# Kernel tuning notes

Measured on AMD Instinct MI355X. Metric: run time of the kernel, lower is better.

The kernel has to match this reference:

```python
import jax, jax.numpy as jnp
import numpy as np

N_NODES = 500_000
N_Q = 500_000
H = 8       # heads
MH = 8      # m // heads


def setup_inputs() -> dict:
    key = jax.random.key(0)
    ks = jax.random.split(key, 6)
    q_phi = jax.random.normal(ks[0], (N_Q, H, MH), dtype=jnp.float32)
    phi_k_pos = jax.random.normal(ks[1], (H, MH, N_NODES), dtype=jnp.float32)
    phi_k_neg = jax.random.normal(ks[2], (H, MH, N_NODES), dtype=jnp.float32)
    # degrees are nonnegative counts accumulated in build(); simulate with scaled uniforms
    deg_pos = jax.random.uniform(ks[3], (N_NODES, H), dtype=jnp.float32) * 32.0
    deg_neg = jax.random.uniform(ks[4], (N_NODES, H), dtype=jnp.float32) * 32.0
    k_indices = jax.random.randint(ks[5], (N_Q,), 0, N_NODES)
    return {
        "q_phi": q_phi,
        "phi_k_pos": phi_k_pos,
        "phi_k_neg": phi_k_neg,
        "deg_pos": deg_pos,
        "deg_neg": deg_neg,
        "k_indices": k_indices,
    }


def reference(q_phi, phi_k_pos, phi_k_neg, deg_pos, deg_neg, k_indices):
    # gather cached per-node random-feature sums: [h, mh, Nq] -> [Nq, h, mh]
    pk_pos = jnp.transpose(phi_k_pos[:, :, k_indices], (2, 0, 1))
    pk_neg = jnp.transpose(phi_k_neg[:, :, k_indices], (2, 0, 1))
    # per-head dot product over the feature chunk
    num_pos = jnp.sum(q_phi * pk_pos, axis=-1)  # [Nq, h]
    num_neg = jnp.sum(q_phi * pk_neg, axis=-1)  # [Nq, h]
    # degree-normalize with clamp_min(1)
    den_pos = jnp.maximum(deg_pos[k_indices], 1.0)  # [Nq, h]
    den_neg = jnp.maximum(deg_neg[k_indices], 1.0)
    return (num_pos / den_pos, num_neg / den_neg)
```

## Files before the change

### kernel.cpp

```cpp
#include <hip/hip_runtime.h>
#include <hip/hip_bf16.h>

constexpr int N_NODES = 500000;
constexpr int N_Q     = 500000;
constexpr int H       = 8;
constexpr int FEAT    = 64;
constexpr int TILES   = (N_NODES + 63) / 64;

__global__ __launch_bounds__(256) void transpose_pk(
    const float* __restrict__ pk_pos,
    const float* __restrict__ pk_neg,
    float* __restrict__ dst)
{
    __shared__ float lds[64 * 65];
    const int t  = threadIdx.x;
    const int n0 = blockIdx.x * 64;
    const float* src = blockIdx.y ? pk_neg : pk_pos;
    float* d = dst + (size_t)blockIdx.y * (size_t)N_NODES * FEAT;

    {
        const int  n  = t & 63;
        const bool ok = (n0 + n) < N_NODES;
        for (int f = (t >> 6); f < 64; f += 4)
            lds[f * 65 + n] = ok ? src[(size_t)f * N_NODES + n0 + n] : 0.0f;
    }
    __syncthreads();
    {
        const int f  = t & 63;
        const int nb = (t >> 6) * 16;
        for (int r = 0; r < 16; ++r) {
            const int n = nb + r;
            if (n0 + n < N_NODES)
                d[(size_t)(n0 + n) * FEAT + f] = lds[f * 65 + n];
        }
    }
}

__global__ __launch_bounds__(256, 4) void iskde_main_kernel(
    const float* __restrict__ q_phi,
    const float* __restrict__ pk_t,
    const float* __restrict__ deg_pos,
    const float* __restrict__ deg_neg,
    const int*   __restrict__ k_idx,
    float*       __restrict__ out)
{
    const int wave_in_blk = threadIdx.x >> 6;
    const int lane        = threadIdx.x & 63;
    const int q           = blockIdx.x * 4 + wave_in_blk;
    if (q >= N_Q) return;

    const int j = k_idx[q];

    const float qv = q_phi[(size_t)q * FEAT + lane];
    const float pv = pk_t[(size_t)j * FEAT + lane];
    const float nv = pk_t[(size_t)(N_NODES + j) * FEAT + lane];

    float sp = qv * pv;
    float sn = qv * nv;

    sp += __shfl_xor(sp, 1, 64);
    sn += __shfl_xor(sn, 1, 64);
    sp += __shfl_xor(sp, 2, 64);
    sn += __shfl_xor(sn, 2, 64);
    sp += __shfl_xor(sp, 4, 64);
    sn += __shfl_xor(sn, 4, 64);

    if ((lane & 7) == 0) {
        const int h = lane >> 3;
        const float dp = fmaxf(deg_pos[(size_t)j * H + h], 1.0f);
        const float dn = fmaxf(deg_neg[(size_t)j * H + h], 1.0f);
        const size_t o = (size_t)q * H + h;
        out[o]                   = sp / dp;
        out[(size_t)N_Q * H + o] = sn / dn;
    }
}

__global__ __launch_bounds__(256, 4) void iskde_gather_kernel(
    const float* __restrict__ q_phi,
    const float* __restrict__ pk_pos,
    const float* __restrict__ pk_neg,
    const float* __restrict__ deg_pos,
    const float* __restrict__ deg_neg,
    const int*   __restrict__ k_idx,
    float*       __restrict__ out)
{
    const int wave_in_blk = threadIdx.x >> 6;
    const int lane        = threadIdx.x & 63;
    const int q           = blockIdx.x * 4 + wave_in_blk;
    if (q >= N_Q) return;

    const int j = k_idx[q];
    const float qv = q_phi[(size_t)q * FEAT + lane];
    const size_t col = (size_t)lane * (size_t)N_NODES + (size_t)j;
    const float pv = pk_pos[col];
    const float nv = pk_neg[col];

    float sp = qv * pv;
    float sn = qv * nv;
    sp += __shfl_xor(sp, 1, 64);
    sn += __shfl_xor(sn, 1, 64);
    sp += __shfl_xor(sp, 2, 64);
    sn += __shfl_xor(sn, 2, 64);
    sp += __shfl_xor(sp, 4, 64);
    sn += __shfl_xor(sn, 4, 64);

    if ((lane & 7) == 0) {
        const int h = lane >> 3;
        const float dp = fmaxf(deg_pos[(size_t)j * H + h], 1.0f);
        const float dn = fmaxf(deg_neg[(size_t)j * H + h], 1.0f);
        const size_t o = (size_t)q * H + h;
        out[o]                   = sp / dp;
        out[(size_t)N_Q * H + o] = sn / dn;
    }
}

extern "C" void kernel_launch(void* const* d_in, const int* in_sizes, int n_in,
                              void* d_out, int out_size, void* d_ws, size_t ws_size,
                              hipStream_t stream) {
    const float* q_phi   = (const float*)d_in[0];
    const float* pk_pos  = (const float*)d_in[1];
    const float* pk_neg  = (const float*)d_in[2];
    const float* deg_pos = (const float*)d_in[3];
    const float* deg_neg = (const float*)d_in[4];
    const int*   k_idx   = (const int*)d_in[5];
    float*       out     = (float*)d_out;

    const size_t need = (size_t)2 * N_NODES * FEAT * sizeof(float);

    if (ws_size >= need) {
        float* pk_t = (float*)d_ws;
        dim3 tgrid(TILES, 2);
        transpose_pk<<<tgrid, 256, 0, stream>>>(pk_pos, pk_neg, pk_t);

        const int blocks = (N_Q + 3) / 4;
        iskde_main_kernel<<<blocks, 256, 0, stream>>>(
            q_phi, pk_t, deg_pos, deg_neg, k_idx, out);
    } else {
        const int blocks = (N_Q + 3) / 4;
        iskde_gather_kernel<<<blocks, 256, 0, stream>>>(
            q_phi, pk_pos, pk_neg, deg_pos, deg_neg, k_idx, out);
    }
}
```

Measured before the change: 531.4 us.

## Vectorize transpose and map one thread per query-head in main kernel

The transpose kernel now reads global memory as float4 along nodes and writes float4 along features, replacing scalar accesses. The main kernel moves from one wave per query with shuffle reductions to one thread per (query, head), computing each 8-element dot product with two float4 loads per operand. Outputs are written with nontemporal stores and fully coalesced. The block count assumes N_Q*H divides by 256 with no bounds check, and the LDS reads in the transpose may now hit more bank conflicts.

Result: faster. 450.6 us (-15.2%).

```diff
diff --git a/kernel.cpp b/kernel.cpp
--- a/kernel.cpp
+++ b/kernel.cpp
@@ -18,25 +18,46 @@
     const float* src = blockIdx.y ? pk_neg : pk_pos;
     float* d = dst + (size_t)blockIdx.y * (size_t)N_NODES * FEAT;
 
+    const int nrem = N_NODES - n0;
+
     {
-        const int  n  = t & 63;
-        const bool ok = (n0 + n) < N_NODES;
-        for (int f = (t >> 6); f < 64; f += 4)
-            lds[f * 65 + n] = ok ? src[(size_t)f * N_NODES + n0 + n] : 0.0f;
+        const int n4 = (t & 15) * 4;
+        const int fb = t >> 4;
+        for (int it = 0; it < 4; ++it) {
+            const int f = fb + it * 16;
+            float4 v = make_float4(0.f, 0.f, 0.f, 0.f);
+            const float* s = src + (size_t)f * N_NODES + n0 + n4;
+            if (n4 + 3 < nrem) {
+                v = *(const float4*)s;
+            } else if (n4 < nrem) {
+                v.x = s[0];
+                if (n4 + 1 < nrem) v.y = s[1];
+                if (n4 + 2 < nrem) v.z = s[2];
+            }
+            float* l = &lds[f * 65 + n4];
+            l[0] = v.x; l[1] = v.y; l[2] = v.z; l[3] = v.w;
+        }
     }
     __syncthreads();
+
     {
-        const int f  = t & 63;
-        const int nb = (t >> 6) * 16;
-        for (int r = 0; r < 16; ++r) {
-            const int n = nb + r;
-            if (n0 + n < N_NODES)
-                d[(size_t)(n0 + n) * FEAT + f] = lds[f * 65 + n];
+        const int f4 = (t & 15) * 4;
+        const int nb = t >> 4;
+        for (int it = 0; it < 4; ++it) {
+            const int n = nb + it * 16;
+            if (n < nrem) {
+                float4 v;
+                v.x = lds[(f4 + 0) * 65 + n];
+                v.y = lds[(f4 + 1) * 65 + n];
+                v.z = lds[(f4 + 2) * 65 + n];
+                v.w = lds[(f4 + 3) * 65 + n];
+                *(float4*)(d + (size_t)(n0 + n) * FEAT + f4) = v;
+            }
         }
     }
 }
 
-__global__ __launch_bounds__(256, 4) void iskde_main_kernel(
+__global__ __launch_bounds__(256) void iskde_main2(
     const float* __restrict__ q_phi,
     const float* __restrict__ pk_t,
     const float* __restrict__ deg_pos,
@@ -44,35 +65,30 @@
     const int*   __restrict__ k_idx,
     float*       __restrict__ out)
 {
-    const int wave_in_blk = threadIdx.x >> 6;
-    const int lane        = threadIdx.x & 63;
-    const int q           = blockIdx.x * 4 + wave_in_blk;
-    if (q >= N_Q) return;
+    const int i = blockIdx.x * 256 + threadIdx.x;
+    const int q = i >> 3;
+    const int h = i & 7;
 
     const int j = k_idx[q];
 
-    const float qv = q_phi[(size_t)q * FEAT + lane];
-    const float pv = pk_t[(size_t)j * FEAT + lane];
-    const float nv = pk_t[(size_t)(N_NODES + j) * FEAT + lane];
+    const float4* qp = (const float4*)(q_phi + (size_t)q * FEAT + h * 8);
+    const float4* pp = (const float4*)(pk_t + (size_t)j * FEAT + h * 8);
+    const float4* pn = (const float4*)(pk_t + ((size_t)N_NODES + (size_t)j) * FEAT + h * 8);
 
-    float sp = qv * pv;
-    float sn = qv * nv;
+    const float4 a0 = qp[0], a1 = qp[1];
+    const float4 b0 = pp[0], b1 = pp[1];
+    const float4 c0 = pn[0], c1 = pn[1];
 
-    sp += __shfl_xor(sp, 1, 64);
-    sn += __shfl_xor(sn, 1, 64);
-    sp += __shfl_xor(sp, 2, 64);
-    sn += __shfl_xor(sn, 2, 64);
-    sp += __shfl_xor(sp, 4, 64);
-    sn += __shfl_xor(sn, 4, 64);
+    float sp = a0.x*b0.x + a0.y*b0.y + a0.z*b0.z + a0.w*b0.w
+             + a1.x*b1.x + a1.y*b1.y + a1.z*b1.z + a1.w*b1.w;
+    float sn = a0.x*c0.x + a0.y*c0.y + a0.z*c0.z + a0.w*c0.w
+             + a1.x*c1.x + a1.y*c1.y + a1.z*c1.z + a1.w*c1.w;
 
-    if ((lane & 7) == 0) {
-        const int h = lane >> 3;
-        const float dp = fmaxf(deg_pos[(size_t)j * H + h], 1.0f);
-        const float dn = fmaxf(deg_neg[(size_t)j * H + h], 1.0f);
-        const size_t o = (size_t)q * H + h;
-        out[o]                   = sp / dp;
-        out[(size_t)N_Q * H + o] = sn / dn;
-    }
+    const float dp = fmaxf(deg_pos[(size_t)j * H + h], 1.0f);
+    const float dn = fmaxf(deg_neg[(size_t)j * H + h], 1.0f);
+
+    __builtin_nontemporal_store(sp / dp, &out[i]);
+    __builtin_nontemporal_store(sn / dn, &out[(size_t)N_Q * H + i]);
 }
 
 __global__ __launch_bounds__(256, 4) void iskde_gather_kernel(
@@ -132,8 +148,8 @@
         dim3 tgrid(TILES, 2);
         transpose_pk<<<tgrid, 256, 0, stream>>>(pk_pos, pk_neg, pk_t);
 
-        const int blocks = (N_Q + 3) / 4;
-        iskde_main_kernel<<<blocks, 256, 0, stream>>>(
+        const int blocks = (N_Q * H) / 256;
+        iskde_main2<<<blocks, 256, 0, stream>>>(
             q_phi, pk_t, deg_pos, deg_neg, k_idx, out);
     } else {
         const int blocks = (N_Q + 3) / 4;
```
